# Optimization experiments

Measured on AMD Instinct MI355X. Metric: run time of the kernel, lower is better.

The kernel has to match this reference:

```python
import jax, jax.numpy as jnp
import numpy as np

D_MODEL = 512
N_HEADS = 8
D_K = D_MODEL // N_HEADS


def setup_inputs() -> dict:
    key = jax.random.key(0)
    ks = jax.random.split(key, 7)
    s = 1.0 / np.sqrt(D_MODEL)
    return {
        "x": jax.random.normal(ks[0], (2, 4096, D_MODEL), dtype=jnp.float32),
        "W_q": jax.random.normal(ks[1], (D_MODEL, D_MODEL), dtype=jnp.float32) * s,
        "W_k": jax.random.normal(ks[2], (D_MODEL, D_MODEL), dtype=jnp.float32) * s,
        "W_v": jax.random.normal(ks[3], (D_MODEL, D_MODEL), dtype=jnp.float32) * s,
        "b_v": jax.random.normal(ks[4], (D_MODEL,), dtype=jnp.float32) * s,
        "W_o": jax.random.normal(ks[5], (D_MODEL, D_MODEL), dtype=jnp.float32) * s,
        "b_o": jax.random.normal(ks[6], (D_MODEL,), dtype=jnp.float32) * s,
    }


def _split_heads(t):
    # [N, S, d_model] -> [N, H, S, d_k]
    N, S, _ = t.shape
    return t.reshape(N, S, N_HEADS, D_K).transpose(0, 2, 1, 3)


def reference(x, W_q, W_k, W_v, b_v, W_o, b_o):
    N, S, _ = x.shape
    # nn.Linear computes x @ W.T (+ b)
    Q = _split_heads(x @ W_q.T)
    K = _split_heads(x @ W_k.T)
    V = _split_heads(x @ W_v.T + b_v)
    scale = jnp.sqrt(jnp.asarray(D_K, x.dtype))
    scores = jnp.einsum('nhqd,nhkd->nhqk', Q, K) / scale  # [N,H,S,S]
    causal = jnp.tril(jnp.ones((S, S), dtype=bool))
    scores = jnp.where(causal, scores, -jnp.inf)
    attn = jax.nn.softmax(scores, axis=-1)
    out = jnp.einsum('nhqk,nhkd->nhqd', attn, V)  # [N,H,S,d_k]
    out = out.transpose(0, 2, 1, 3).reshape(N, S, D_MODEL)
    return out @ W_o.T + b_o
```

## Files before the change

### kernel.cpp

```cpp
#include <hip/hip_runtime.h>
#include <hip/hip_bf16.h>

#define NB 2
#define SEQ 4096
#define DM 512
#define NH 8
#define DKH 64
#define MTOT (NB*SEQ)

typedef __attribute__((ext_vector_type(4))) float f32x4;
typedef __attribute__((ext_vector_type(16))) float f32x16;
typedef __attribute__((ext_vector_type(8))) short bf16x8;
typedef __attribute__((ext_vector_type(2))) unsigned uint2v;

__device__ inline unsigned short f2bf(float f) {
    union { float f; unsigned int u; } v; v.f = f;
    unsigned int r = v.u + 0x7FFFu + ((v.u >> 16) & 1u);
    return (unsigned short)(r >> 16);
}

#define QSCALE 0.18033688011112042f

__global__ void cast_kernel(const float* __restrict__ x, const float* __restrict__ wq,
                            const float* __restrict__ wk, const float* __restrict__ wv,
                            const float* __restrict__ wo, unsigned short* __restrict__ dst) {
    const int NX = MTOT*DM;
    const int NW = DM*DM;
    int i4 = blockIdx.x * blockDim.x + threadIdx.x;
    long e = (long)i4 * 4;
    if (e >= NX + 4L*NW) return;
    const float* src; long off;
    if (e < NX)           { src = x;  off = e; }
    else if (e < NX+NW)   { src = wq; off = e - NX; }
    else if (e < NX+2*NW) { src = wk; off = e - NX - NW; }
    else if (e < NX+3*NW) { src = wv; off = e - NX - 2*NW; }
    else                  { src = wo; off = e - NX - 3*NW; }
    float4 v = *reinterpret_cast<const float4*>(src + off);
    ushort4 o;
    o.x = f2bf(v.x); o.y = f2bf(v.y); o.z = f2bf(v.z); o.w = f2bf(v.w);
    *reinterpret_cast<ushort4*>(dst + e) = o;
}

template<int MODE>
__global__ __launch_bounds__(256, 2) void gemm_bt(
    const unsigned short* __restrict__ A,
    const unsigned short* __restrict__ B,
    const float* __restrict__ bias,
    unsigned short* __restrict__ Qh, unsigned short* __restrict__ Kh,
    unsigned short* __restrict__ Vt,
    float* __restrict__ Cout)
{
    const int K = 512;
    __shared__ __align__(16) unsigned short As[128*64];
    __shared__ __align__(16) unsigned short Bs[128*64];
    int tid = threadIdx.x;
    int wid = tid >> 6, lane = tid & 63;
    int wr = wid >> 1, wc = wid & 1;
    int brow = blockIdx.x * 128;
    int bcol = blockIdx.y * 128;
    int l15 = lane & 15, l4 = lane >> 4;

    f32x4 acc[4][4] = {};

    for (int kt = 0; kt < K/64; ++kt) {
        __syncthreads();
        #pragma unroll
        for (int i = 0; i < 4; ++i) {
            int rbase = i*32 + wid*8;
            int row = rbase + (lane >> 3);
            int csrc = (lane & 7) ^ (row & 7);
            const unsigned short* asrc = A + (long)(brow+row)*K + kt*64 + csrc*8;
            __builtin_amdgcn_global_load_lds(
                (const __attribute__((address_space(1))) unsigned int*)asrc,
                (__attribute__((address_space(3))) unsigned int*)&As[rbase*64], 16, 0, 0);
            const unsigned short* bsrc = B + (long)(bcol+row)*K + kt*64 + csrc*8;
            __builtin_amdgcn_global_load_lds(
                (const __attribute__((address_space(1))) unsigned int*)bsrc,
                (__attribute__((address_space(3))) unsigned int*)&Bs[rbase*64], 16, 0, 0);
        }
        __syncthreads();
        #pragma unroll
        for (int kk = 0; kk < 2; ++kk) {
            bf16x8 af[4], bfr[4];
            #pragma unroll
            for (int mi = 0; mi < 4; ++mi) {
                int row = wr*64 + mi*16 + l15;
                int colb = (kk*32 + l4*8) * 2;
                af[mi] = *reinterpret_cast<const bf16x8*>(
                    reinterpret_cast<const char*>(As) + row*128 + (colb ^ ((row&7)<<4)));
            }
            #pragma unroll
            for (int ni = 0; ni < 4; ++ni) {
                int row = wc*64 + ni*16 + l15;
                int colb = (kk*32 + l4*8) * 2;
                bfr[ni] = *reinterpret_cast<const bf16x8*>(
                    reinterpret_cast<const char*>(Bs) + row*128 + (colb ^ ((row&7)<<4)));
            }
            #pragma unroll
            for (int mi = 0; mi < 4; ++mi)
                #pragma unroll
                for (int ni = 0; ni < 4; ++ni)
                    acc[mi][ni] = __builtin_amdgcn_mfma_f32_16x16x32_bf16(af[mi], bfr[ni], acc[mi][ni], 0, 0, 0);
        }
    }

    #pragma unroll
    for (int mi = 0; mi < 4; ++mi) {
        #pragma unroll
        for (int ni = 0; ni < 4; ++ni) {
            #pragma unroll
            for (int r = 0; r < 4; ++r) {
                int row = brow + wr*64 + mi*16 + l4*4 + r;
                int col = bcol + wc*64 + ni*16 + l15;
                float v = acc[mi][ni][r];
                if (MODE == 0) {
                    int which = col >> 9;
                    int cw = col & 511;
                    int h = cw >> 6, d = cw & 63;
                    int b = row >> 12, s = row & 4095;
                    int bh = b*NH + h;
                    if (which == 0) {
                        Qh[((long)(bh*SEQ + s))*DKH + d] = f2bf(v * QSCALE);
                    } else if (which == 1) {
                        Kh[((long)(bh*SEQ + s))*DKH + d] = f2bf(v);
                    } else {
                        Vt[((long)(bh*DKH + d))*SEQ + s] = f2bf(v + bias[cw]);
                    }
                } else {
                    Cout[(long)row*DM + col] = v + bias[col];
                }
            }
        }
    }
}

__global__ __launch_bounds__(256, 2) void attn_kernel(
    const unsigned short* __restrict__ Qh,
    const unsigned short* __restrict__ Kh,
    const unsigned short* __restrict__ Vt,
    unsigned short* __restrict__ Obf)
{
    __shared__ __align__(16) unsigned short Klds[2][2][64*64];
    __shared__ __align__(16) unsigned short Vlds[2][2][64*64];
    const int tid = threadIdx.x;
    const int wid = tid >> 6, lane = tid & 63;
    const int g = wid & 1, p = wid >> 1;
    const int l31 = lane & 31;
    const int hi  = lane >> 5;
    const int bh  = blockIdx.x;
    const int j   = blockIdx.y;

    const unsigned short* Qbase = Qh + (long)bh*SEQ*DKH;
    const unsigned short* Kbase = Kh + (long)bh*SEQ*DKH;
    const unsigned short* Vbase = Vt + (long)bh*DKH*SEQ;

    const int swz = (l31 & 7) << 4;

    auto STAGE1 = [&](int pb, int b, int key0) {
        #pragma unroll
        for (int ii = 0; ii < 2; ++ii) {
            const int rbase = wid*16 + ii*8;
            const int row = rbase + (lane >> 3);
            const int ck = (lane & 7) ^ (row & 7);
            const unsigned short* ksrc = Kbase + (long)(key0 + row)*DKH + ck*8;
            __builtin_amdgcn_global_load_lds(
                (const __attribute__((address_space(1))) unsigned int*)ksrc,
                (__attribute__((address_space(3))) unsigned int*)&Klds[pb][b][rbase*64], 16, 0, 0);
            const unsigned short* vsrc = Vbase + (long)row*SEQ + key0 + ck*8;
            __builtin_amdgcn_global_load_lds(
                (const __attribute__((address_space(1))) unsigned int*)vsrc,
                (__attribute__((address_space(3))) unsigned int*)&Vlds[pb][b][rbase*64], 16, 0, 0);
        }
    };

    #pragma unroll 1
    for (int half = 0; half < 2; ++half) {
        const int tile = half ? (int)j : 63 - (int)j;
        const int q0w = tile*64 + g*32;
        const int q   = q0w + l31;
        const int nss = (tile >> 1) + 1;

        bf16x8 qf[4];
        #pragma unroll
        for (int kk = 0; kk < 4; ++kk)
            qf[kk] = *reinterpret_cast<const bf16x8*>(Qbase + (long)q*DKH + kk*16 + hi*8);

        float m = -1e30f, lsum = 0.f;
        f32x16 od0 = {}, od1 = {};

        STAGE1(0, 0, 0);
        if (tile >= 1) STAGE1(1, 0, 64);
        __syncthreads();

        #pragma unroll 1
        for (int ss = 0; ss < nss; ++ss) {
            const int nb = (ss + 1) & 1;
            if (2*(ss+1)     <= tile) STAGE1(0, nb, (2*(ss+1))     << 6);
            if (2*(ss+1) + 1 <= tile) STAGE1(1, nb, (2*(ss+1) + 1) << 6);

            const int kb = 2*ss + p;
            if (kb <= tile) {
                const int key0 = kb << 6;
                const char* kl = reinterpret_cast<const char*>(&Klds[p][ss & 1][0]);
                const char* vl = reinterpret_cast<const char*>(&Vlds[p][ss & 1][0]);

                bf16x8 kfr[4][2];
                #pragma unroll
                for (int kk = 0; kk < 4; ++kk) {
                    const int co = (kk*32 + hi*16) ^ swz;
                    kfr[kk][0] = *reinterpret_cast<const bf16x8*>(kl + l31*128      + co);
                    kfr[kk][1] = *reinterpret_cast<const bf16x8*>(kl + (32+l31)*128 + co);
                }
                f32x16 s0 = {}, s1 = {};
                __builtin_amdgcn_s_setprio(1);
                #pragma unroll
                for (int kk = 0; kk < 4; ++kk) {
                    s0 = __builtin_amdgcn_mfma_f32_32x32x16_bf16(kfr[kk][0], qf[kk], s0, 0, 0, 0);
                    s1 = __builtin_amdgcn_mfma_f32_32x32x16_bf16(kfr[kk][1], qf[kk], s1, 0, 0, 0);
                }
                __builtin_amdgcn_s_setprio(0);

                if (kb == tile) {
                    #pragma unroll
                    for (int r = 0; r < 16; ++r) {
                        const int ko = (r&3) + 8*(r>>2) + 4*hi;
                        if (key0 + ko > q)      s0[r] = -1e30f;
                        if (key0 + 32 + ko > q) s1[r] = -1e30f;
                    }
                }

                float pmax = s0[0];
                #pragma unroll
                for (int r = 1; r < 16; ++r) pmax = fmaxf(pmax, s0[r]);
                #pragma unroll
                for (int r = 0; r < 16; ++r) pmax = fmaxf(pmax, s1[r]);
                {
                    uint2v pr = __builtin_amdgcn_permlane32_swap(__float_as_uint(pmax), __float_as_uint(pmax), false, false);
                    pmax = fmaxf(__uint_as_float(pr[0]), __uint_as_float(pr[1]));
                }
                if (__any(pmax > m + 6.0f)) {
                    const float mn = fmaxf(m, pmax);
                    const float alpha = __builtin_amdgcn_exp2f(m - mn);
                    m = mn;
                    lsum *= alpha;
                    #pragma unroll
                    for (int r = 0; r < 16; ++r) { od0[r] *= alpha; od1[r] *= alpha; }
                }

                float rsc0 = 0.f, rsc1 = 0.f;
#define EXP_CHUNK(SV, RS) do {                                                     \
                _Pragma("unroll")                                                  \
                for (int r = 0; r < 16; ++r) {                                     \
                    SV[r] = __builtin_amdgcn_exp2f(SV[r] - m);                     \
                    RS += SV[r];                                                   \
                } } while (0)

#define PV_STEP(SV, VLS, KS, B0) do {                                              \
                unsigned c0, c1, c2, c3;                                           \
                float t0 = SV[B0+0], t1 = SV[B0+1], t2 = SV[B0+2], t3 = SV[B0+3];  \
                float t4 = SV[B0+4], t5 = SV[B0+5], t6 = SV[B0+6], t7 = SV[B0+7];  \
                asm("v_cvt_pk_bf16_f32 %0, %1, %2" : "=v"(c0) : "v"(t0), "v"(t1)); \
                asm("v_cvt_pk_bf16_f32 %0, %1, %2" : "=v"(c1) : "v"(t2), "v"(t3)); \
                asm("v_cvt_pk_bf16_f32 %0, %1, %2" : "=v"(c2) : "v"(t4), "v"(t5)); \
                asm("v_cvt_pk_bf16_f32 %0, %1, %2" : "=v"(c3) : "v"(t6), "v"(t7)); \
                uint2v sw0 = __builtin_amdgcn_permlane32_swap(c0, c2, false, false); \
                uint2v sw1 = __builtin_amdgcn_permlane32_swap(c1, c3, false, false); \
                union { unsigned u[4]; bf16x8 v; } pu;                             \
                pu.u[0] = sw0[0]; pu.u[1] = sw1[0]; pu.u[2] = sw0[1]; pu.u[3] = sw1[1]; \
                bf16x8 vf0 = *reinterpret_cast<const bf16x8*>(VLS + l31*128      + (((KS)*32 + hi*16) ^ swz)); \
                od0 = __builtin_amdgcn_mfma_f32_32x32x16_bf16(vf0, pu.v, od0, 0, 0, 0); \
                bf16x8 vf1 = *reinterpret_cast<const bf16x8*>(VLS + (32+l31)*128 + (((KS)*32 + hi*16) ^ swz)); \
                od1 = __builtin_amdgcn_mfma_f32_32x32x16_bf16(vf1, pu.v, od1, 0, 0, 0); \
            } while (0)

                __builtin_amdgcn_s_setprio(1);
                EXP_CHUNK(s0, rsc0);
                PV_STEP(s0, vl, 0, 0);
                PV_STEP(s0, vl, 1, 8);
                EXP_CHUNK(s1, rsc1);
                PV_STEP(s1, vl, 2, 0);
                PV_STEP(s1, vl, 3, 8);
                __builtin_amdgcn_s_setprio(0);
#undef PV_STEP
#undef EXP_CHUNK
                lsum += rsc0 + rsc1;
            }
            __syncthreads();
        }

        char*  sod = reinterpret_cast<char*>(&Klds[g][0][0]);
        float* sml = reinterpret_cast<float*>(&Klds[g][1][0]);
        const int lswz = (lane & 7) << 4;
        if (p == 1) {
            #pragma unroll
            for (int i = 0; i < 4; ++i) {
                *reinterpret_cast<f32x4*>(sod + lane*128 + ((i*16) ^ lswz)) =
                    (f32x4){od0[i*4+0], od0[i*4+1], od0[i*4+2], od0[i*4+3]};
                *reinterpret_cast<f32x4*>(sod + lane*128 + (((i+4)*16) ^ lswz)) =
                    (f32x4){od1[i*4+0], od1[i*4+1], od1[i*4+2], od1[i*4+3]};
            }
            sml[lane*2]     = m;
            sml[lane*2 + 1] = lsum;
        }
        __syncthreads();
        if (p == 0) {
            const float pm  = sml[lane*2];
            const float plv = sml[lane*2 + 1];
            const float mn = fmaxf(m, pm);
            const float a0 = __builtin_amdgcn_exp2f(m - mn);
            const float a1 = __builtin_amdgcn_exp2f(pm - mn);
            lsum = lsum*a0 + plv*a1;
            #pragma unroll
            for (int i = 0; i < 4; ++i) {
                f32x4 t0 = *reinterpret_cast<const f32x4*>(sod + lane*128 + ((i*16) ^ lswz));
                f32x4 t1 = *reinterpret_cast<const f32x4*>(sod + lane*128 + (((i+4)*16) ^ lswz));
                #pragma unroll
                for (int k = 0; k < 4; ++k) {
                    od0[i*4+k] = od0[i*4+k]*a0 + t0[k]*a1;
                    od1[i*4+k] = od1[i*4+k]*a0 + t1[k]*a1;
                }
            }
            {
                uint2v pr = __builtin_amdgcn_permlane32_swap(__float_as_uint(lsum), __float_as_uint(lsum), false, false);
                lsum = __uint_as_float(pr[0]) + __uint_as_float(pr[1]);
            }
            const float rls = 1.0f / lsum;
            const long obase = (long)((bh >> 3)*SEQ + q)*DM + (bh & 7)*DKH;
            #pragma unroll
            for (int rr = 0; rr < 4; ++rr) {
                ushort4 w0, w1;
                w0.x = f2bf(od0[rr*4+0]*rls); w0.y = f2bf(od0[rr*4+1]*rls);
                w0.z = f2bf(od0[rr*4+2]*rls); w0.w = f2bf(od0[rr*4+3]*rls);
                *reinterpret_cast<ushort4*>(Obf + obase + rr*8 + hi*4) = w0;
                w1.x = f2bf(od1[rr*4+0]*rls); w1.y = f2bf(od1[rr*4+1]*rls);
                w1.z = f2bf(od1[rr*4+2]*rls); w1.w = f2bf(od1[rr*4+3]*rls);
                *reinterpret_cast<ushort4*>(Obf + obase + 32 + rr*8 + hi*4) = w1;
            }
        }
        __syncthreads();
    }
}

extern "C" void kernel_launch(void* const* d_in, const int* in_sizes, int n_in,
                              void* d_out, int out_size, void* d_ws, size_t ws_size,
                              hipStream_t stream) {
    const float* x  = (const float*)d_in[0];
    const float* wq = (const float*)d_in[1];
    const float* wk = (const float*)d_in[2];
    const float* wv = (const float*)d_in[3];
    const float* bv = (const float*)d_in[4];
    const float* wo = (const float*)d_in[5];
    const float* bo = (const float*)d_in[6];
    float* out = (float*)d_out;

    unsigned short* ws = (unsigned short*)d_ws;
    unsigned short* Xbf  = ws;
    unsigned short* Wqkv = Xbf  + 4194304;
    unsigned short* Wob  = Wqkv + 786432;
    unsigned short* Qh   = Wob  + 262144;
    unsigned short* Kh   = Qh   + 4194304;
    unsigned short* Vt   = Kh   + 4194304;
    unsigned short* Obf  = Vt   + 4194304;

    cast_kernel<<<5120, 256, 0, stream>>>(x, wq, wk, wv, wo, Xbf);

    dim3 g1(64, 12);
    gemm_bt<0><<<g1, 256, 0, stream>>>(Xbf, Wqkv, bv, Qh, Kh, Vt, nullptr);

    dim3 g2(16, 32);
    attn_kernel<<<g2, 256, 0, stream>>>(Qh, Kh, Vt, Obf);

    dim3 g3(64, 4);
    gemm_bt<1><<<g3, 256, 0, stream>>>(Obf, Wob, bo, nullptr, nullptr, nullptr, out);
}
```

Before: 110.1 us.

## Split causal attention across two key partitions with a separate merge kernel

Adds an attention kernel that splits each query tile's causal key range into two interleaved partitions (even/odd key tiles). Each partition runs in its own block and writes a partial bf16 output plus max and sum. A new merge kernel combines the partials into the final O. This raises the block count to 2048 with a 4-blocks-per-CU launch bound, aiming for better occupancy and load balance across the causal triangle. The cost is an extra launch and the round trip of the partial buffers through memory. The old kernel is kept as a fallback when the workspace is too small; its exp and PV interleaving was also reordered.

```diff
diff --git a/kernel.cpp b/kernel.cpp
--- a/kernel.cpp
+++ b/kernel.cpp
@@ -17,6 +17,9 @@
     union { float f; unsigned int u; } v; v.f = f;
     unsigned int r = v.u + 0x7FFFu + ((v.u >> 16) & 1u);
     return (unsigned short)(r >> 16);
+}
+__device__ inline float bf2f(unsigned short u) {
+    union { unsigned int v; float f; } x; x.v = ((unsigned int)u) << 16; return x.f;
 }
 
 #define QSCALE 0.18033688011112042f
@@ -134,7 +137,232 @@
     }
 }
 
-__global__ __launch_bounds__(256, 2) void attn_kernel(
+#define PV_STEP_M(SV, VLS, KS, B0, OD0, OD1)  do {                                 \
+        unsigned c0, c1, c2, c3;                                                   \
+        float t0 = SV[B0+0], t1 = SV[B0+1], t2 = SV[B0+2], t3 = SV[B0+3];          \
+        float t4 = SV[B0+4], t5 = SV[B0+5], t6 = SV[B0+6], t7 = SV[B0+7];          \
+        asm("v_cvt_pk_bf16_f32 %0, %1, %2" : "=v"(c0) : "v"(t0), "v"(t1));         \
+        asm("v_cvt_pk_bf16_f32 %0, %1, %2" : "=v"(c1) : "v"(t2), "v"(t3));         \
+        asm("v_cvt_pk_bf16_f32 %0, %1, %2" : "=v"(c2) : "v"(t4), "v"(t5));         \
+        asm("v_cvt_pk_bf16_f32 %0, %1, %2" : "=v"(c3) : "v"(t6), "v"(t7));         \
+        uint2v sw0 = __builtin_amdgcn_permlane32_swap(c0, c2, false, false);       \
+        uint2v sw1 = __builtin_amdgcn_permlane32_swap(c1, c3, false, false);       \
+        union { unsigned u[4]; bf16x8 v; } pu;                                     \
+        pu.u[0] = sw0[0]; pu.u[1] = sw1[0]; pu.u[2] = sw0[1]; pu.u[3] = sw1[1];    \
+        bf16x8 vf0 = *reinterpret_cast<const bf16x8*>(VLS + l31*128      + (((KS)*32 + hi*16) ^ swz)); \
+        OD0 = __builtin_amdgcn_mfma_f32_32x32x16_bf16(vf0, pu.v, OD0, 0, 0, 0);    \
+        bf16x8 vf1 = *reinterpret_cast<const bf16x8*>(VLS + (32+l31)*128 + (((KS)*32 + hi*16) ^ swz)); \
+        OD1 = __builtin_amdgcn_mfma_f32_32x32x16_bf16(vf1, pu.v, OD1, 0, 0, 0);    \
+    } while (0)
+
+__global__ __launch_bounds__(256, 4) void attn_split(
+    const unsigned short* __restrict__ Qh,
+    const unsigned short* __restrict__ Kh,
+    const unsigned short* __restrict__ Vt,
+    unsigned short* __restrict__ pO0, unsigned short* __restrict__ pO1,
+    float* __restrict__ pml)
+{
+    __shared__ __align__(16) unsigned short Kc[2][64*64];
+    __shared__ __align__(16) unsigned short Vc[2][64*64];
+    const int tid = threadIdx.x;
+    const int wid = tid >> 6, lane = tid & 63;
+    const int g = wid & 1, p = wid >> 1;
+    const int l31 = lane & 31;
+    const int hi  = lane >> 5;
+
+    const int id   = blockIdx.x;
+    const int xcd  = id & 7;
+    const int rest = id >> 3;
+    const int bh   = xcd + ((rest & 1) << 3);
+    const int rem  = rest >> 1;
+    const int t    = 63 - (rem >> 1);
+    const int c    = rem & 1;
+
+    const unsigned short* Qbase = Qh + (long)bh*SEQ*DKH;
+    const unsigned short* Kbase = Kh + (long)bh*SEQ*DKH;
+    const unsigned short* Vbase = Vt + (long)bh*DKH*SEQ;
+
+    const int q0w = t*64 + g*32;
+    const int q   = q0w + l31;
+    const int nu  = (t >= c) ? (((t - c) >> 1) + 1) : 0;
+    const int swz = (l31 & 7) << 4;
+
+    bf16x8 qf[4];
+    #pragma unroll
+    for (int kk = 0; kk < 4; ++kk)
+        qf[kk] = *reinterpret_cast<const bf16x8*>(Qbase + (long)q*DKH + kk*16 + hi*8);
+
+    auto STAGE = [&](int b, int key0) {
+        #pragma unroll
+        for (int ii = 0; ii < 2; ++ii) {
+            const int rbase = wid*16 + ii*8;
+            const int row = rbase + (lane >> 3);
+            const int ck = (lane & 7) ^ (row & 7);
+            const unsigned short* ksrc = Kbase + (long)(key0 + row)*DKH + ck*8;
+            __builtin_amdgcn_global_load_lds(
+                (const __attribute__((address_space(1))) unsigned int*)ksrc,
+                (__attribute__((address_space(3))) unsigned int*)&Kc[b][rbase*64], 16, 0, 0);
+            const unsigned short* vsrc = Vbase + (long)row*SEQ + key0 + ck*8;
+            __builtin_amdgcn_global_load_lds(
+                (const __attribute__((address_space(1))) unsigned int*)vsrc,
+                (__attribute__((address_space(3))) unsigned int*)&Vc[b][rbase*64], 16, 0, 0);
+        }
+    };
+
+    float m = -1e30f, lsum = 0.f;
+    f32x16 od0 = {}, od1 = {};
+
+    if (nu > 0) STAGE(0, c << 6);
+    __syncthreads();
+    int cur = 0;
+
+    #pragma unroll 1
+    for (int s = 0; s < nu; ++s) {
+        const int u = c + 2*s;
+        if (s + 1 < nu) STAGE(cur ^ 1, (u + 2) << 6);
+        const char* kl = reinterpret_cast<const char*>(&Kc[cur][0]) + p*32*128;
+        const char* vl = reinterpret_cast<const char*>(&Vc[cur][0]);
+
+        bf16x8 kfr[4];
+        #pragma unroll
+        for (int kk = 0; kk < 4; ++kk)
+            kfr[kk] = *reinterpret_cast<const bf16x8*>(kl + l31*128 + ((kk*32 + hi*16) ^ swz));
+        f32x16 sv = {};
+        __builtin_amdgcn_s_setprio(1);
+        #pragma unroll
+        for (int kk = 0; kk < 4; ++kk)
+            sv = __builtin_amdgcn_mfma_f32_32x32x16_bf16(kfr[kk], qf[kk], sv, 0, 0, 0);
+        __builtin_amdgcn_s_setprio(0);
+
+        if (u == t) {
+            const int kbase = (u << 6) + (p << 5);
+            #pragma unroll
+            for (int r = 0; r < 16; ++r) {
+                const int ko = (r&3) + 8*(r>>2) + 4*hi;
+                if (kbase + ko > q) sv[r] = -1e30f;
+            }
+        }
+
+        float m0 = fmaxf(sv[0],  fmaxf(sv[1],  sv[2]));
+        float m1 = fmaxf(sv[3],  fmaxf(sv[4],  sv[5]));
+        float m2 = fmaxf(sv[6],  fmaxf(sv[7],  sv[8]));
+        float m3 = fmaxf(sv[9],  fmaxf(sv[10], sv[11]));
+        float m4 = fmaxf(sv[12], fmaxf(sv[13], sv[14]));
+        float pmax = fmaxf(fmaxf(m0, fmaxf(m1, m2)), fmaxf(sv[15], fmaxf(m3, m4)));
+        {
+            uint2v pr = __builtin_amdgcn_permlane32_swap(__float_as_uint(pmax), __float_as_uint(pmax), false, false);
+            pmax = fmaxf(__uint_as_float(pr[0]), __uint_as_float(pr[1]));
+        }
+        if (__any(pmax > m + 6.0f)) {
+            const float mn = fmaxf(m, pmax);
+            const float alpha = __builtin_amdgcn_exp2f(m - mn);
+            m = mn;
+            lsum *= alpha;
+            #pragma unroll
+            for (int r = 0; r < 16; ++r) { od0[r] *= alpha; od1[r] *= alpha; }
+        }
+
+        float rs = 0.f;
+        #pragma unroll
+        for (int r = 0; r < 16; ++r) {
+            sv[r] = __builtin_amdgcn_exp2f(sv[r] - m);
+            rs += sv[r];
+        }
+        lsum += rs;
+
+        __builtin_amdgcn_s_setprio(1);
+        PV_STEP_M(sv, vl, (2*p),     0, od0, od1);
+        PV_STEP_M(sv, vl, (2*p + 1), 8, od0, od1);
+        __builtin_amdgcn_s_setprio(0);
+
+        __syncthreads();
+        cur ^= 1;
+    }
+
+    char*  sod = reinterpret_cast<char*>(&Kc[g][0]);
+    float* sml = reinterpret_cast<float*>(&Vc[g][0]);
+    const int lswz = (lane & 7) << 4;
+    if (p == 1) {
+        #pragma unroll
+        for (int i = 0; i < 4; ++i) {
+            *reinterpret_cast<f32x4*>(sod + lane*128 + ((i*16) ^ lswz)) =
+                (f32x4){od0[i*4+0], od0[i*4+1], od0[i*4+2], od0[i*4+3]};
+            *reinterpret_cast<f32x4*>(sod + lane*128 + (((i+4)*16) ^ lswz)) =
+                (f32x4){od1[i*4+0], od1[i*4+1], od1[i*4+2], od1[i*4+3]};
+        }
+        sml[lane*2]     = m;
+        sml[lane*2 + 1] = lsum;
+    }
+    __syncthreads();
+    if (p == 0) {
+        const float pm  = sml[lane*2];
+        const float plv = sml[lane*2 + 1];
+        const float mn = fmaxf(m, pm);
+        const float a0 = __builtin_amdgcn_exp2f(m - mn);
+        const float a1 = __builtin_amdgcn_exp2f(pm - mn);
+        m = mn;
+        lsum = lsum*a0 + plv*a1;
+        #pragma unroll
+        for (int i = 0; i < 4; ++i) {
+            f32x4 t0 = *reinterpret_cast<const f32x4*>(sod + lane*128 + ((i*16) ^ lswz));
+            f32x4 t1 = *reinterpret_cast<const f32x4*>(sod + lane*128 + (((i+4)*16) ^ lswz));
+            #pragma unroll
+            for (int k = 0; k < 4; ++k) {
+                od0[i*4+k] = od0[i*4+k]*a0 + t0[k]*a1;
+                od1[i*4+k] = od1[i*4+k]*a0 + t1[k]*a1;
+            }
+        }
+        {
+            uint2v pr = __builtin_amdgcn_permlane32_swap(__float_as_uint(lsum), __float_as_uint(lsum), false, false);
+            lsum = __uint_as_float(pr[0]) + __uint_as_float(pr[1]);
+        }
+        const int rowg = (bh << 12) + (t << 6) + (g << 5) + l31;
+        unsigned short* pO = (c ? pO1 : pO0) + (long)rowg*64;
+        #pragma unroll
+        for (int rr = 0; rr < 4; ++rr) {
+            ushort4 w0, w1;
+            w0.x = f2bf(od0[rr*4+0]); w0.y = f2bf(od0[rr*4+1]);
+            w0.z = f2bf(od0[rr*4+2]); w0.w = f2bf(od0[rr*4+3]);
+            *reinterpret_cast<ushort4*>(pO + rr*8 + hi*4) = w0;
+            w1.x = f2bf(od1[rr*4+0]); w1.y = f2bf(od1[rr*4+1]);
+            w1.z = f2bf(od1[rr*4+2]); w1.w = f2bf(od1[rr*4+3]);
+            *reinterpret_cast<ushort4*>(pO + 32 + rr*8 + hi*4) = w1;
+        }
+        if (hi == 0) {
+            float* base = pml + c*131072;
+            base[rowg]         = m;
+            base[65536 + rowg] = lsum;
+        }
+    }
+}
+
+__global__ __launch_bounds__(256) void merge_o(
+    const unsigned short* __restrict__ pO0, const unsigned short* __restrict__ pO1,
+    const float* __restrict__ pml, unsigned short* __restrict__ Obf)
+{
+    const int tg  = blockIdx.x * 256 + threadIdx.x;
+    const int row = tg >> 3;
+    const int db  = (tg & 7) * 8;
+    const float m0 = pml[row],          l0 = pml[65536 + row];
+    const float m1 = pml[131072 + row], l1 = pml[131072 + 65536 + row];
+    const float mn = fmaxf(m0, m1);
+    const float a0 = __builtin_amdgcn_exp2f(m0 - mn);
+    const float a1 = __builtin_amdgcn_exp2f(m1 - mn);
+    const float rls = 1.0f / (l0*a0 + l1*a1);
+    const float w0 = a0 * rls, w1 = a1 * rls;
+    bf16x8 v0 = *reinterpret_cast<const bf16x8*>(pO0 + (long)row*64 + db);
+    bf16x8 v1 = *reinterpret_cast<const bf16x8*>(pO1 + (long)row*64 + db);
+    const int bh = row >> 12, s = row & 4095;
+    const long tok = ((long)(bh >> 3) << 12) + s;
+    const int col = ((bh & 7) << 6) + db;
+    union { unsigned short u[8]; bf16x8 v; } out;
+    #pragma unroll
+    for (int k = 0; k < 8; ++k)
+        out.u[k] = f2bf(bf2f((unsigned short)v0[k])*w0 + bf2f((unsigned short)v1[k])*w1);
+    *reinterpret_cast<bf16x8*>(Obf + tok*DM + col) = out.v;
+}
+
+__global__ __launch_bounds__(256, 2) void attn_r9(
     const unsigned short* __restrict__ Qh,
     const unsigned short* __restrict__ Kh,
     const unsigned short* __restrict__ Vt,
@@ -153,7 +381,6 @@
     const unsigned short* Qbase = Qh + (long)bh*SEQ*DKH;
     const unsigned short* Kbase = Kh + (long)bh*SEQ*DKH;
     const unsigned short* Vbase = Vt + (long)bh*DKH*SEQ;
-
     const int swz = (l31 & 7) << 4;
 
     auto STAGE1 = [&](int pb, int b, int key0) {
@@ -247,43 +474,19 @@
                     for (int r = 0; r < 16; ++r) { od0[r] *= alpha; od1[r] *= alpha; }
                 }
 
-                float rsc0 = 0.f, rsc1 = 0.f;
-#define EXP_CHUNK(SV, RS) do {                                                     \
-                _Pragma("unroll")                                                  \
-                for (int r = 0; r < 16; ++r) {                                     \
-                    SV[r] = __builtin_amdgcn_exp2f(SV[r] - m);                     \
-                    RS += SV[r];                                                   \
-                } } while (0)
-
-#define PV_STEP(SV, VLS, KS, B0) do {                                              \
-                unsigned c0, c1, c2, c3;                                           \
-                float t0 = SV[B0+0], t1 = SV[B0+1], t2 = SV[B0+2], t3 = SV[B0+3];  \
-                float t4 = SV[B0+4], t5 = SV[B0+5], t6 = SV[B0+6], t7 = SV[B0+7];  \
-                asm("v_cvt_pk_bf16_f32 %0, %1, %2" : "=v"(c0) : "v"(t0), "v"(t1)); \
-                asm("v_cvt_pk_bf16_f32 %0, %1, %2" : "=v"(c1) : "v"(t2), "v"(t3)); \
-                asm("v_cvt_pk_bf16_f32 %0, %1, %2" : "=v"(c2) : "v"(t4), "v"(t5)); \
-                asm("v_cvt_pk_bf16_f32 %0, %1, %2" : "=v"(c3) : "v"(t6), "v"(t7)); \
-                uint2v sw0 = __builtin_amdgcn_permlane32_swap(c0, c2, false, false); \
-                uint2v sw1 = __builtin_amdgcn_permlane32_swap(c1, c3, false, false); \
-                union { unsigned u[4]; bf16x8 v; } pu;                             \
-                pu.u[0] = sw0[0]; pu.u[1] = sw1[0]; pu.u[2] = sw0[1]; pu.u[3] = sw1[1]; \
-                bf16x8 vf0 = *reinterpret_cast<const bf16x8*>(VLS + l31*128      + (((KS)*32 + hi*16) ^ swz)); \
-                od0 = __builtin_amdgcn_mfma_f32_32x32x16_bf16(vf0, pu.v, od0, 0, 0, 0); \
-                bf16x8 vf1 = *reinterpret_cast<const bf16x8*>(VLS + (32+l31)*128 + (((KS)*32 + hi*16) ^ swz)); \
-                od1 = __builtin_amdgcn_mfma_f32_32x32x16_bf16(vf1, pu.v, od1, 0, 0, 0); \
-            } while (0)
+                float rs = 0.f;
+                #pragma unroll
+                for (int r = 0; r < 16; ++r) { s0[r] = __builtin_amdgcn_exp2f(s0[r] - m); rs += s0[r]; }
+                #pragma unroll
+                for (int r = 0; r < 16; ++r) { s1[r] = __builtin_amdgcn_exp2f(s1[r] - m); rs += s1[r]; }
+                lsum += rs;
 
                 __builtin_amdgcn_s_setprio(1);
-                EXP_CHUNK(s0, rsc0);
-                PV_STEP(s0, vl, 0, 0);
-                PV_STEP(s0, vl, 1, 8);
-                EXP_CHUNK(s1, rsc1);
-                PV_STEP(s1, vl, 2, 0);
-                PV_STEP(s1, vl, 3, 8);
+                PV_STEP_M(s0, vl, 0, 0, od0, od1);
+                PV_STEP_M(s0, vl, 1, 8, od0, od1);
+                PV_STEP_M(s1, vl, 2, 0, od0, od1);
+                PV_STEP_M(s1, vl, 3, 8, od0, od1);
                 __builtin_amdgcn_s_setprio(0);
-#undef PV_STEP
-#undef EXP_CHUNK
-                lsum += rsc0 + rsc1;
             }
             __syncthreads();
         }
@@ -361,14 +564,24 @@
     unsigned short* Kh   = Qh   + 4194304;
     unsigned short* Vt   = Kh   + 4194304;
     unsigned short* Obf  = Vt   + 4194304;
+    unsigned short* pO0  = Obf  + 4194304;
+    unsigned short* pO1  = pO0  + 4194304;
+    float*          pml  = (float*)(pO1 + 4194304);
+
+    const size_t needed = (size_t)(22020096 + 8388608) * 2 + (size_t)262144 * 4;
 
     cast_kernel<<<5120, 256, 0, stream>>>(x, wq, wk, wv, wo, Xbf);
 
     dim3 g1(64, 12);
     gemm_bt<0><<<g1, 256, 0, stream>>>(Xbf, Wqkv, bv, Qh, Kh, Vt, nullptr);
 
-    dim3 g2(16, 32);
-    attn_kernel<<<g2, 256, 0, stream>>>(Qh, Kh, Vt, Obf);
+    if (ws_size >= needed) {
+        attn_split<<<2048, 256, 0, stream>>>(Qh, Kh, Vt, pO0, pO1, pml);
+        merge_o<<<2048, 256, 0, stream>>>(pO0, pO1, pml, Obf);
+    } else {
+        dim3 g2(16, 32);
+        attn_r9<<<g2, 256, 0, stream>>>(Qh, Kh, Vt, Obf);
+    }
 
     dim3 g3(64, 4);
     gemm_bt<1><<<g3, 256, 0, stream>>>(Obf, Wob, bo, nullptr, nullptr, nullptr, out);
```

After: 112.6 us. 2.2% more time.
